# Kernel tuning notes

Hardware: AMD Instinct MI355X
Metric: run time of the kernel (lower is better)

The kernel has to match this reference:

```python
import jax, jax.numpy as jnp
import numpy as np

B, N, EMB, POS_EMB, ENC_DIM, NCLS, L = 256, 32, 128, 64, 256, 2, 4
EDGE_DIM = 2 * NCLS + 1            # one-hot(src) + one-hot(dst) + distance
IN_DIM = EMB + POS_EMB + 1         # enc_emb + pos_emb + numAgents_emb


def _w(k, shape):
    return jax.random.normal(k, shape, jnp.float32) / np.float32(np.sqrt(shape[-1]))


def setup_inputs() -> dict:
    key = jax.random.key(0)
    ks = jax.random.split(key, 16)
    return {
        "pos": jax.random.normal(ks[0], (B, N, 2), jnp.float32),
        "enc": jax.random.normal(ks[1], (B, ENC_DIM), jnp.float32),
        "pos_emb": jax.random.normal(ks[2], (B, N, POS_EMB), jnp.float32),
        "numAgents_emb": jax.random.normal(ks[3], (B, 1), jnp.float32),
        "T": jax.random.randint(ks[4], (B, N), 0, NCLS),
        "num_agents": N,
        # decoder_fc: Linear(ENC_DIM, EMB//2) -> Tanh -> Linear(EMB//2, EMB)
        "fc1_w": _w(ks[5], (EMB // 2, ENC_DIM)), "fc1_b": jnp.zeros((EMB // 2,), jnp.float32),
        "fc2_w": _w(ks[6], (EMB, EMB // 2)), "fc2_b": jnp.zeros((EMB,), jnp.float32),
        # lin_in: Linear(IN_DIM, EMB)
        "lin_w": _w(ks[7], (EMB, IN_DIM)), "lin_b": jnp.zeros((EMB,), jnp.float32),
        # per-layer message MLP: Linear(2*EMB+EDGE_DIM, EMB) -> Tanh -> Linear(EMB, EMB) -> Tanh
        "msg_w1": _w(ks[8], (L, EMB, 2 * EMB + EDGE_DIM)), "msg_b1": jnp.zeros((L, EMB), jnp.float32),
        "msg_w2": _w(ks[9], (L, EMB, EMB)), "msg_b2": jnp.zeros((L, EMB), jnp.float32),
        # per-layer update MLP: Linear(2*EMB, EMB) -> Tanh -> Linear(EMB, EMB) -> Tanh
        "upd_w1": _w(ks[10], (L, EMB, 2 * EMB)), "upd_b1": jnp.zeros((L, EMB), jnp.float32),
        "upd_w2": _w(ks[11], (L, EMB, EMB)), "upd_b2": jnp.zeros((L, EMB), jnp.float32),
    }


def reference(pos, enc, pos_emb, numAgents_emb, T, num_agents,
              fc1_w, fc1_b, fc2_w, fc2_b, lin_w, lin_b,
              msg_w1, msg_b1, msg_w2, msg_b2,
              upd_w1, upd_b1, upd_w2, upd_b2):
    b, n = pos.shape[0], num_agents
    # decoder_fc on scene encoding, broadcast to every agent (dropout in eval = identity)
    e = jnp.tanh(enc @ fc1_w.T + fc1_b) @ fc2_w.T + fc2_b            # (B, EMB)
    enc_emb = jnp.broadcast_to(e[:, None, :], (b, n, e.shape[-1]))
    na_emb = jnp.broadcast_to(numAgents_emb[:, None, :], (b, n, 1))
    x = jnp.concatenate([pos_emb, na_emb, enc_emb], axis=-1).reshape(b * n, -1)  # (B*N, IN_DIM)

    # fully connected edges per graph, batch-offset node ids
    row = jnp.repeat(jnp.arange(n), n)        # edge_index[0] = source j
    col = jnp.tile(jnp.arange(n), n)          # edge_index[1] = target i
    off = (jnp.arange(b) * n)[:, None]
    e_src = (row[None, :] + off).reshape(-1)  # (E,) with E = B*N^2
    e_dst = (col[None, :] + off).reshape(-1)

    # edge attributes: class one-hots of both endpoints + euclidean distance
    t_unique = jnp.arange(NCLS)
    T_oh = (T.reshape(-1)[:, None] == t_unique[None, :]).astype(jnp.float32)  # (B*N, NCLS)
    pf = pos.reshape(-1, 2)
    dist = jnp.sqrt(jnp.sum((pf[e_src] - pf[e_dst]) ** 2, axis=-1, keepdims=True))
    edge_attr = jnp.concatenate([T_oh[e_src], T_oh[e_dst], dist], axis=-1)     # (E, EDGE_DIM)

    # SocialInterDecGNN: lin_in, then L residual MPNN layers with add-aggregation
    h = x @ lin_w.T + lin_b
    for l in range(msg_w1.shape[0]):
        m_in = jnp.concatenate([h[e_dst], h[e_src], edge_attr], axis=-1)  # [h_i, h_j, e]
        m = jnp.tanh(jnp.tanh(m_in @ msg_w1[l].T + msg_b1[l]) @ msg_w2[l].T + msg_b2[l])
        aggr = jax.ops.segment_sum(m, e_dst, num_segments=b * n)          # scatter-add at target
        u_in = jnp.concatenate([h, aggr], axis=-1)
        h = h + jnp.tanh(jnp.tanh(u_in @ upd_w1[l].T + upd_b1[l]) @ upd_w2[l].T + upd_b2[l])
    return h  # (B*N, EMB)
```

## Files before the change

kernel.cpp:

```cpp
#include <hip/hip_runtime.h>

#define NN   32
#define EMB  128
#define PEMB 64
#define ENCD 256
#define NLAY 4
#define W1C  261
#define IND  193
#define UPAD 132
#define TSCALE 2.885390081777927f

typedef __attribute__((ext_vector_type(8))) short short8;
typedef __attribute__((ext_vector_type(4))) float floatx4;

__device__ unsigned short g_wC_h[16384 * 8], g_wC_l[16384 * 8];
__device__ unsigned short g_wD_h[8192 * 8],  g_wD_l[8192 * 8];
__device__ unsigned short g_wE1_h[16384 * 8], g_wE1_l[16384 * 8];
__device__ unsigned short g_wE2_h[8192 * 8],  g_wE2_l[8192 * 8];

__device__ __forceinline__ float fast_tanh(float x) {
  float e = __expf(2.0f * x);
  return 1.0f - __fdividef(2.0f, e + 1.0f);
}
__device__ __forceinline__ float tanh2(float s) {
  float e;
  asm("v_exp_f32 %0, %1" : "=v"(e) : "v"(s));
  const float ep1 = e + 1.0f;
  float r;
  asm("v_rcp_f32 %0, %1" : "=v"(r) : "v"(ep1));
  return __builtin_fmaf(-2.0f, r, 1.0f);
}
__device__ __forceinline__ unsigned short f2bf(float x) {
  unsigned u = __float_as_uint(x);
  return (unsigned short)((u + 0x7fffu + ((u >> 16) & 1u)) >> 16);
}
__device__ __forceinline__ float bf2f(unsigned short h) {
  return __uint_as_float(((unsigned)h) << 16);
}
__device__ __forceinline__ unsigned cvtpk(float a, float b) {
  unsigned r;
  asm("v_cvt_pk_bf16_f32 %0, %1, %2" : "=v"(r) : "v"(a), "v"(b));
  return r;
}

__device__ __forceinline__ floatx4 mfma3(short8 ah, short8 al, short8 bh, short8 bl, floatx4 acc) {
  acc = __builtin_amdgcn_mfma_f32_16x16x32_bf16(ah, bh, acc, 0, 0, 0);
  acc = __builtin_amdgcn_mfma_f32_16x16x32_bf16(al, bh, acc, 0, 0, 0);
  acc = __builtin_amdgcn_mfma_f32_16x16x32_bf16(ah, bl, acc, 0, 0, 0);
  return acc;
}

__device__ __forceinline__ void cvt_plane(const float (*src)[UPAD],
                                          unsigned short (*dH)[64][8],
                                          unsigned short (*dL)[64][8],
                                          int p, int lane) {
  const int row  = (lane & 15) + ((p & 1) << 4);
  const int koff = ((p >> 1) << 5) + ((lane >> 4) << 3);
  float x[8];
  *(float4*)&x[0] = *(const float4*)&src[row][koff];
  *(float4*)&x[4] = *(const float4*)&src[row][koff + 4];
  unsigned h[4], lo[4];
  #pragma unroll
  for (int q = 0; q < 4; q++) {
    h[q] = cvtpk(x[2*q], x[2*q+1]);
    const float r0 = x[2*q]   - __uint_as_float(h[q] << 16);
    const float r1 = x[2*q+1] - __uint_as_float(h[q] & 0xffff0000u);
    lo[q] = cvtpk(r0, r1);
  }
  *(uint4*)&dH[p][lane][0] = make_uint4(h[0], h[1], h[2], h[3]);
  *(uint4*)&dL[p][lane][0] = make_uint4(lo[0], lo[1], lo[2], lo[3]);
}

__device__ __forceinline__ short8 build_t(const float* uv, const float* vv,
                                          float d, const float* c5q) {
  float t[8];
  #pragma unroll
  for (int m = 0; m < 8; m++) t[m] = tanh2(uv[m] + vv[m] + d * c5q[m]);
  uint4 p = make_uint4(cvtpk(t[0], t[1]), cvtpk(t[2], t[3]),
                       cvtpk(t[4], t[5]), cvtpk(t[6], t[7]));
  return *(short8*)&p;
}

__device__ __forceinline__ float dot16_lds(const float* base, const float* wreg) {
  const float4 a = *(const float4*)(base);
  const float4 b = *(const float4*)(base + 4);
  const float4 c = *(const float4*)(base + 8);
  const float4 d = *(const float4*)(base + 12);
  return a.x*wreg[0] + a.y*wreg[1] + a.z*wreg[2]  + a.w*wreg[3]
       + b.x*wreg[4] + b.y*wreg[5] + b.z*wreg[6]  + b.w*wreg[7]
       + c.x*wreg[8] + c.y*wreg[9] + c.z*wreg[10] + c.w*wreg[11]
       + d.x*wreg[12]+ d.y*wreg[13]+ d.z*wreg[14] + d.w*wreg[15];
}

__global__ __launch_bounds__(256) void wconv(
    const float* __restrict__ msg_w1, const float* __restrict__ msg_w2,
    const float* __restrict__ upd_w1, const float* __restrict__ upd_w2) {
  const int t = blockIdx.x * 256 + threadIdx.x;
  const float* src;
  unsigned short *dh, *dl;
  if (t < 16384) {
    const int lane = t & 63, ks = (t >> 6) & 3, tile = (t >> 8) & 15, l = t >> 12;
    src = msg_w1 + l * EMB * W1C + (((tile & 7) << 4) + (lane & 15)) * W1C
        + (tile >> 3) * EMB + ks * 32 + ((lane >> 4) << 3);
    dh = g_wC_h + t * 8; dl = g_wC_l + t * 8;
  } else if (t < 24576) {
    const int r = t - 16384;
    const int lane = r & 63, ks = (r >> 6) & 3, ct = (r >> 8) & 7, l = r >> 11;
    src = msg_w2 + l * EMB * EMB + ((ct << 4) + (lane & 15)) * EMB + ks * 32 + ((lane >> 4) << 3);
    dh = g_wD_h + r * 8; dl = g_wD_l + r * 8;
  } else if (t < 40960) {
    const int r = t - 24576;
    const int lane = r & 63, ks = (r >> 6) & 7, ct = (r >> 9) & 7, l = r >> 12;
    src = upd_w1 + l * EMB * 2 * EMB + ((ct << 4) + (lane & 15)) * 2 * EMB + ks * 32 + ((lane >> 4) << 3);
    dh = g_wE1_h + r * 8; dl = g_wE1_l + r * 8;
  } else if (t < 49152) {
    const int r = t - 40960;
    const int lane = r & 63, ks = (r >> 6) & 3, ct = (r >> 8) & 7, l = r >> 11;
    src = upd_w2 + l * EMB * EMB + ((ct << 4) + (lane & 15)) * EMB + ks * 32 + ((lane >> 4) << 3);
    dh = g_wE2_h + r * 8; dl = g_wE2_l + r * 8;
  } else return;
  unsigned short hh[8], ll[8];
  #pragma unroll
  for (int m = 0; m < 8; m++) {
    const float x = src[m] * TSCALE;
    const unsigned short hb = f2bf(x);
    hh[m] = hb;
    ll[m] = f2bf(x - bf2f(hb));
  }
  *(short8*)dh = *(const short8*)hh;
  *(short8*)dl = *(const short8*)ll;
}

__global__ __launch_bounds__(1024)
__attribute__((amdgpu_waves_per_eu(4, 4)))
void fsd_fused(
    const float* __restrict__ pos, const float* __restrict__ enc,
    const float* __restrict__ pos_emb, const float* __restrict__ na_emb,
    const int* __restrict__ T,
    const float* __restrict__ fc1_w, const float* __restrict__ fc1_b,
    const float* __restrict__ fc2_w, const float* __restrict__ fc2_b,
    const float* __restrict__ lin_w, const float* __restrict__ lin_b,
    const float* __restrict__ msg_w1, const float* __restrict__ msg_b1,
    const float* __restrict__ msg_b2,
    const float* __restrict__ upd_b1, const float* __restrict__ upd_b2,
    float* __restrict__ out)
{
  __shared__ __align__(16) float h32[NN][UPAD];
  __shared__ __align__(16) float u_s[NN][UPAD];
  __shared__ __align__(16) float v_s[NN][UPAD];
  __shared__ __align__(16) unsigned short hfH[8][64][8],  hfL[8][64][8];
  __shared__ __align__(16) unsigned short agfH[8][64][8], agfL[8][64][8];
  __shared__ __align__(16) unsigned short w2fH[8][4][64][8], w2fL[8][4][64][8];
  __shared__ float e_s[EMB];
  __shared__ float c5_s[EMB];
  __shared__ float b2m_s[EMB];
  __shared__ float clsU[2][EMB], clsV[2][EMB];
  __shared__ float enc_s[ENCD];
  __shared__ float hidA_s[64];
  __shared__ float posx_s[NN], posy_s[NN];
  __shared__ int   T_s[NN];

  const int b    = blockIdx.x;
  const int tid  = threadIdx.x;
  const int w    = tid >> 6, lane = tid & 63;
  const int o    = tid & 127, g8 = tid >> 7;
  const int l15  = lane & 15, l4 = lane >> 4;

  if (tid < ENCD) enc_s[tid] = enc[b * ENCD + tid];
  if (tid < NN) {
    posx_s[tid] = pos[(b * NN + tid) * 2 + 0];
    posy_s[tid] = pos[(b * NN + tid) * 2 + 1];
    T_s[tid]    = T[b * NN + tid];
  }
  __syncthreads();
  if (tid < 64) {
    float a = fc1_b[tid];
    const float* wr = fc1_w + tid * ENCD;
    #pragma unroll 8
    for (int k = 0; k < ENCD; k++) a += enc_s[k] * wr[k];
    hidA_s[tid] = fast_tanh(a);
  }
  __syncthreads();
  if (tid < EMB) {
    float a = fc2_b[tid];
    const float* wr = fc2_w + tid * 64;
    #pragma unroll 8
    for (int k = 0; k < 64; k++) a += hidA_s[k] * wr[k];
    e_s[tid] = a;
  }
  float* pe_s = &u_s[0][0];
  for (int idx = tid; idx < NN * PEMB; idx += 1024)
    pe_s[idx] = pos_emb[b * NN * PEMB + idx];
  __syncthreads();

  {
    const float nav = na_emb[b];
    const float* wr = lin_w + o * IND;
    float ebias = lin_b[o] + nav * wr[PEMB];
    #pragma unroll 8
    for (int k = 0; k < EMB; k++) ebias += e_s[k] * wr[65 + k];
    float acc[4];
    #pragma unroll
    for (int n = 0; n < 4; n++) acc[n] = ebias;
    for (int kc = 0; kc < PEMB; kc += 16) {
      float wreg[16];
      #pragma unroll
      for (int q = 0; q < 16; q++) wreg[q] = wr[kc + q];
      #pragma unroll
      for (int n = 0; n < 4; n++)
        acc[n] += dot16_lds(&pe_s[(g8 + 8 * n) * PEMB + kc], wreg);
    }
    __syncthreads();
    #pragma unroll
    for (int n = 0; n < 4; n++) h32[g8 + 8 * n][o] = acc[n];
  }
  __syncthreads();
  if (w < 8) cvt_plane(h32, hfH, hfL, w, lane);
  __syncthreads();

  for (int l = 0; l < NLAY; l++) {
    const float* b1  = msg_b1 + l * EMB;
    const float* b2  = msg_b2 + l * EMB;
    const float* ub1 = upd_b1 + l * EMB;
    const float* ub2 = upd_b2 + l * EMB;
    const float* w1  = msg_w1 + l * EMB * W1C;

    if (tid < EMB) { c5_s[tid] = w1[tid * W1C + 260] * TSCALE; b2m_s[tid] = b2[tid] * TSCALE; }
    {
      const int c = (tid >> 7) & 1, oo = tid & 127;
      if (tid < 256)      clsU[c][oo] = (b1[oo] + w1[oo * W1C + 258 + c]) * TSCALE;
      else if (tid < 512) clsV[c][oo] = w1[oo * W1C + 256 + c] * TSCALE;
    }
    {
      const unsigned short* sH = g_wD_h + l * 16384;
      const unsigned short* sL = g_wD_l + l * 16384;
      unsigned short* dH = &w2fH[0][0][0][0];
      unsigned short* dL = &w2fL[0][0][0][0];
      for (int idx = tid; idx < 2048; idx += 1024) {
        *(short8*)(dH + idx * 8) = *(const short8*)(sH + idx * 8);
        *(short8*)(dL + idx * 8) = *(const short8*)(sL + idx * 8);
      }
    }
    __syncthreads();

    {
      const int part = w >> 3;
      const int col  = ((w & 7) << 4) + l15;
      floatx4 acc0 = {0.f,0.f,0.f,0.f}, acc1 = {0.f,0.f,0.f,0.f};
      #pragma unroll
      for (int ks = 0; ks < 4; ks++) {
        const int idx = (((l * 16 + w) * 4 + ks) * 64 + lane) * 8;
        const short8 bh = *(const short8*)(g_wC_h + idx);
        const short8 bl = *(const short8*)(g_wC_l + idx);
        const short8 ah0 = *(const short8*)&hfH[ks*2+0][lane][0];
        const short8 al0 = *(const short8*)&hfL[ks*2+0][lane][0];
        const short8 ah1 = *(const short8*)&hfH[ks*2+1][lane][0];
        const short8 al1 = *(const short8*)&hfL[ks*2+1][lane][0];
        acc0 = mfma3(ah0, al0, bh, bl, acc0);
        acc1 = mfma3(ah1, al1, bh, bl, acc1);
      }
      float (*dst)[UPAD] = part ? v_s : u_s;
      const float (*tab)[EMB] = part ? clsV : clsU;
      #pragma unroll
      for (int q = 0; q < 4; q++) {
        const int r0 = (l4 << 2) + q;
        const int r1 = r0 + 16;
        dst[r0][col] = acc0[q] + tab[T_s[r0]][col];
        dst[r1][col] = acc1[q] + tab[T_s[r1]][col];
      }
    }
    __syncthreads();

    {
      #pragma unroll 1
      for (int ii = 0; ii < 2; ii++) {
        const int i = (w << 1) + ii;
        const float pix = posx_s[i], piy = posy_s[i];
        float psum[8];
        #pragma unroll
        for (int ct = 0; ct < 8; ct++) psum[ct] = 0.f;

        #pragma unroll 1
        for (int jt = 0; jt < 2; jt++) {
          const int jr = l15 + (jt << 4);
          const float dxx = posx_s[jr] - pix, dyy = posy_s[jr] - piy;
          const float d = sqrtf(dxx * dxx + dyy * dyy);
          floatx4 acc[8];
          #pragma unroll
          for (int ct = 0; ct < 8; ct++) acc[ct] = (floatx4){0.f,0.f,0.f,0.f};

          #pragma unroll 1
          for (int q = 0; q < 4; q++) {
            const int k8 = (q << 5) + (l4 << 3);
            float uv[8], vv[8], c5q[8];
            *(float4*)&uv[0]  = *(const float4*)&u_s[i][k8];
            *(float4*)&uv[4]  = *(const float4*)&u_s[i][k8 + 4];
            *(float4*)&vv[0]  = *(const float4*)&v_s[jr][k8];
            *(float4*)&vv[4]  = *(const float4*)&v_s[jr][k8 + 4];
            *(float4*)&c5q[0] = *(const float4*)&c5_s[k8];
            *(float4*)&c5q[4] = *(const float4*)&c5_s[k8 + 4];
            const short8 aF = build_t(uv, vv, d, c5q);
            #pragma unroll
            for (int ct = 0; ct < 8; ct++) {
              const short8 bh = *(const short8*)&w2fH[ct][q][lane][0];
              const short8 bl = *(const short8*)&w2fL[ct][q][lane][0];
              acc[ct] = __builtin_amdgcn_mfma_f32_16x16x32_bf16(aF, bl, acc[ct], 0, 0, 0);
              acc[ct] = __builtin_amdgcn_mfma_f32_16x16x32_bf16(aF, bh, acc[ct], 0, 0, 0);
            }
          }
          #pragma unroll
          for (int ct = 0; ct < 8; ct++) {
            const float b2c = b2m_s[(ct << 4) + l15];
            #pragma unroll
            for (int q = 0; q < 4; q++)
              psum[ct] += tanh2(acc[ct][q] + b2c);
          }
        }

        #pragma unroll
        for (int ct = 0; ct < 8; ct++) {
          float p = psum[ct];
          p += __shfl_xor(p, 16);
          p += __shfl_xor(p, 32);
          if (lane < 16) {
            const int c     = (ct << 4) + l15;
            const int plane = ((c >> 5) << 1) + (i >> 4);
            const int slot  = (i & 15) + (((c >> 3) & 3) << 4);
            const int elem  = c & 7;
            const unsigned short hb = f2bf(p);
            agfH[plane][slot][elem] = hb;
            agfL[plane][slot][elem] = f2bf(p - bf2f(hb));
          }
        }
      }
    }
    __syncthreads();

    {
      const int ct = w & 7, jt = w >> 3;
      const int col = (ct << 4) + l15;
      const float bo = ub1[col] * TSCALE;
      floatx4 acc = {0.f,0.f,0.f,0.f};
      #pragma unroll
      for (int ks = 0; ks < 8; ks++) {
        const int idx = (((l * 8 + ct) * 8 + ks) * 64 + lane) * 8;
        const short8 bh = *(const short8*)(g_wE1_h + idx);
        const short8 bl = *(const short8*)(g_wE1_l + idx);
        short8 ah, al;
        if (ks < 4) {
          ah = *(const short8*)&hfH[ks*2+jt][lane][0];
          al = *(const short8*)&hfL[ks*2+jt][lane][0];
        } else {
          ah = *(const short8*)&agfH[(ks-4)*2+jt][lane][0];
          al = *(const short8*)&agfL[(ks-4)*2+jt][lane][0];
        }
        acc = mfma3(ah, al, bh, bl, acc);
      }
      #pragma unroll
      for (int q = 0; q < 4; q++) {
        const int r = (jt << 4) + (l4 << 2) + q;
        u_s[r][col] = tanh2(acc[q] + bo);
      }
    }
    __syncthreads();

    if (w < 8) cvt_plane(u_s, agfH, agfL, w, lane);
    __syncthreads();

    {
      const int ct = w & 7, jt = w >> 3;
      const int col = (ct << 4) + l15;
      const float bo = ub2[col] * TSCALE;
      floatx4 acc = {0.f,0.f,0.f,0.f};
      #pragma unroll
      for (int ks = 0; ks < 4; ks++) {
        const int idx = (((l * 8 + ct) * 4 + ks) * 64 + lane) * 8;
        const short8 bh = *(const short8*)(g_wE2_h + idx);
        const short8 bl = *(const short8*)(g_wE2_l + idx);
        const short8 ah = *(const short8*)&agfH[ks*2+jt][lane][0];
        const short8 al = *(const short8*)&agfL[ks*2+jt][lane][0];
        acc = mfma3(ah, al, bh, bl, acc);
      }
      #pragma unroll
      for (int q = 0; q < 4; q++) {
        const int r = (jt << 4) + (l4 << 2) + q;
        h32[r][col] += tanh2(acc[q] + bo);
      }
    }
    __syncthreads();

    if (l + 1 < NLAY) {
      if (w < 8) cvt_plane(h32, hfH, hfL, w, lane);
      __syncthreads();
    }
  }

  for (int idx = tid; idx < NN * EMB; idx += 1024)
    out[b * NN * EMB + idx] = h32[idx >> 7][idx & 127];
}

extern "C" void kernel_launch(void* const* d_in, const int* in_sizes, int n_in,
                              void* d_out, int out_size, void* d_ws, size_t ws_size,
                              hipStream_t stream) {
  const float* pos     = (const float*)d_in[0];
  const float* enc     = (const float*)d_in[1];
  const float* pos_emb = (const float*)d_in[2];
  const float* na_emb  = (const float*)d_in[3];
  const int*   T       = (const int*)d_in[4];
  const float* fc1_w = (const float*)d_in[6];
  const float* fc1_b = (const float*)d_in[7];
  const float* fc2_w = (const float*)d_in[8];
  const float* fc2_b = (const float*)d_in[9];
  const float* lin_w = (const float*)d_in[10];
  const float* lin_b = (const float*)d_in[11];
  const float* msg_w1 = (const float*)d_in[12];
  const float* msg_b1 = (const float*)d_in[13];
  const float* msg_w2 = (const float*)d_in[14];
  const float* msg_b2 = (const float*)d_in[15];
  const float* upd_w1 = (const float*)d_in[16];
  const float* upd_b1 = (const float*)d_in[17];
  const float* upd_w2 = (const float*)d_in[18];
  const float* upd_b2 = (const float*)d_in[19];

  wconv<<<192, 256, 0, stream>>>(msg_w1, msg_w2, upd_w1, upd_w2);
  fsd_fused<<<256, 1024, 0, stream>>>(pos, enc, pos_emb, na_emb, T,
      fc1_w, fc1_b, fc2_w, fc2_b, lin_w, lin_b,
      msg_w1, msg_b1, msg_b2, upd_b1, upd_b2,
      (float*)d_out);
}
```

Measured before the change: 171.0 us.

## Switch edge message second-layer GEMM to 32x32x16 MFMA tiles

Reorganizes the per-edge message MLP second layer to use 32x32x16 bf16 MFMA instead of 16x16x32, with each wave covering all 32 source agents at once. The msg_w2 fragment layout in wconv and in LDS is reordered to match, the tanh-input A fragments are built once per target agent and reused across four output column tiles, and sched_group_barrier hints interleave LDS reads with MFMAs. This is meant to cut redundant A-fragment construction, LDS traffic and the cross-lane reduction. In exchange it holds more registers (16-wide accumulators plus eight A fragments), which may strain occupancy at the fixed waves-per-EU setting.

```diff
diff --git a/kernel.cpp b/kernel.cpp
--- a/kernel.cpp
+++ b/kernel.cpp
@@ -12,6 +12,7 @@
 
 typedef __attribute__((ext_vector_type(8))) short short8;
 typedef __attribute__((ext_vector_type(4))) float floatx4;
+typedef __attribute__((ext_vector_type(16))) float floatx16;
 
 __device__ unsigned short g_wC_h[16384 * 8], g_wC_l[16384 * 8];
 __device__ unsigned short g_wD_h[8192 * 8],  g_wD_l[8192 * 8];
@@ -71,13 +72,20 @@
   *(uint4*)&dL[p][lane][0] = make_uint4(lo[0], lo[1], lo[2], lo[3]);
 }
 
-__device__ __forceinline__ short8 build_t(const float* uv, const float* vv,
-                                          float d, const float* c5q) {
-  float t[8];
-  #pragma unroll
-  for (int m = 0; m < 8; m++) t[m] = tanh2(uv[m] + vv[m] + d * c5q[m]);
-  uint4 p = make_uint4(cvtpk(t[0], t[1]), cvtpk(t[2], t[3]),
-                       cvtpk(t[4], t[5]), cvtpk(t[6], t[7]));
+__device__ __forceinline__ short8 build_t32(const float* us, const float* vs,
+                                            const float* cs, float d) {
+  const float4 u0 = *(const float4*)us, u1 = *(const float4*)(us + 4);
+  const float4 v0 = *(const float4*)vs, v1 = *(const float4*)(vs + 4);
+  const float4 c0 = *(const float4*)cs, c1 = *(const float4*)(cs + 4);
+  const float t0 = tanh2(u0.x + v0.x + d * c0.x);
+  const float t1 = tanh2(u0.y + v0.y + d * c0.y);
+  const float t2 = tanh2(u0.z + v0.z + d * c0.z);
+  const float t3 = tanh2(u0.w + v0.w + d * c0.w);
+  const float t4 = tanh2(u1.x + v1.x + d * c1.x);
+  const float t5 = tanh2(u1.y + v1.y + d * c1.y);
+  const float t6 = tanh2(u1.z + v1.z + d * c1.z);
+  const float t7 = tanh2(u1.w + v1.w + d * c1.w);
+  uint4 p = make_uint4(cvtpk(t0, t1), cvtpk(t2, t3), cvtpk(t4, t5), cvtpk(t6, t7));
   return *(short8*)&p;
 }
 
@@ -105,8 +113,8 @@
     dh = g_wC_h + t * 8; dl = g_wC_l + t * 8;
   } else if (t < 24576) {
     const int r = t - 16384;
-    const int lane = r & 63, ks = (r >> 6) & 3, ct = (r >> 8) & 7, l = r >> 11;
-    src = msg_w2 + l * EMB * EMB + ((ct << 4) + (lane & 15)) * EMB + ks * 32 + ((lane >> 4) << 3);
+    const int lane = r & 63, kt = (r >> 6) & 7, nt = (r >> 9) & 3, l = r >> 11;
+    src = msg_w2 + l * EMB * EMB + ((nt << 5) + (lane & 31)) * EMB + (kt << 4) + ((lane >> 5) << 3);
     dh = g_wD_h + r * 8; dl = g_wD_l + r * 8;
   } else if (t < 40960) {
     const int r = t - 24576;
@@ -150,7 +158,7 @@
   __shared__ __align__(16) float v_s[NN][UPAD];
   __shared__ __align__(16) unsigned short hfH[8][64][8],  hfL[8][64][8];
   __shared__ __align__(16) unsigned short agfH[8][64][8], agfL[8][64][8];
-  __shared__ __align__(16) unsigned short w2fH[8][4][64][8], w2fL[8][4][64][8];
+  __shared__ __align__(16) unsigned short w2fH[4][8][64][8], w2fL[4][8][64][8];
   __shared__ float e_s[EMB];
   __shared__ float c5_s[EMB];
   __shared__ float b2m_s[EMB];
@@ -272,59 +280,52 @@
     __syncthreads();
 
     {
+      const int j32 = lane & 31;
+      const int khi = (lane >> 5) << 3;
+      const float pjx = posx_s[j32], pjy = posy_s[j32];
       #pragma unroll 1
       for (int ii = 0; ii < 2; ii++) {
         const int i = (w << 1) + ii;
-        const float pix = posx_s[i], piy = posy_s[i];
-        float psum[8];
-        #pragma unroll
-        for (int ct = 0; ct < 8; ct++) psum[ct] = 0.f;
+        const float dxx = pjx - posx_s[i], dyy = pjy - posy_s[i];
+        const float d = sqrtf(dxx * dxx + dyy * dyy);
+        const short8 aF0 = build_t32(&u_s[i][  0 + khi], &v_s[j32][  0 + khi], &c5_s[  0 + khi], d);
+        const short8 aF1 = build_t32(&u_s[i][ 16 + khi], &v_s[j32][ 16 + khi], &c5_s[ 16 + khi], d);
+        const short8 aF2 = build_t32(&u_s[i][ 32 + khi], &v_s[j32][ 32 + khi], &c5_s[ 32 + khi], d);
+        const short8 aF3 = build_t32(&u_s[i][ 48 + khi], &v_s[j32][ 48 + khi], &c5_s[ 48 + khi], d);
+        const short8 aF4 = build_t32(&u_s[i][ 64 + khi], &v_s[j32][ 64 + khi], &c5_s[ 64 + khi], d);
+        const short8 aF5 = build_t32(&u_s[i][ 80 + khi], &v_s[j32][ 80 + khi], &c5_s[ 80 + khi], d);
+        const short8 aF6 = build_t32(&u_s[i][ 96 + khi], &v_s[j32][ 96 + khi], &c5_s[ 96 + khi], d);
+        const short8 aF7 = build_t32(&u_s[i][112 + khi], &v_s[j32][112 + khi], &c5_s[112 + khi], d);
 
         #pragma unroll 1
-        for (int jt = 0; jt < 2; jt++) {
-          const int jr = l15 + (jt << 4);
-          const float dxx = posx_s[jr] - pix, dyy = posy_s[jr] - piy;
-          const float d = sqrtf(dxx * dxx + dyy * dyy);
-          floatx4 acc[8];
+        for (int nt = 0; nt < 4; nt++) {
+          floatx16 acc = {0.f,0.f,0.f,0.f,0.f,0.f,0.f,0.f,0.f,0.f,0.f,0.f,0.f,0.f,0.f,0.f};
+          #define DSTEP(kt, aF) { \
+            const short8 bl_ = *(const short8*)&w2fL[nt][kt][lane][0]; \
+            acc = __builtin_amdgcn_mfma_f32_32x32x16_bf16(aF, bl_, acc, 0, 0, 0); \
+            const short8 bh_ = *(const short8*)&w2fH[nt][kt][lane][0]; \
+            acc = __builtin_amdgcn_mfma_f32_32x32x16_bf16(aF, bh_, acc, 0, 0, 0); }
+          DSTEP(0, aF0) DSTEP(1, aF1) DSTEP(2, aF2) DSTEP(3, aF3)
+          DSTEP(4, aF4) DSTEP(5, aF5) DSTEP(6, aF6) DSTEP(7, aF7)
+          #undef DSTEP
           #pragma unroll
-          for (int ct = 0; ct < 8; ct++) acc[ct] = (floatx4){0.f,0.f,0.f,0.f};
-
-          #pragma unroll 1
-          for (int q = 0; q < 4; q++) {
-            const int k8 = (q << 5) + (l4 << 3);
-            float uv[8], vv[8], c5q[8];
-            *(float4*)&uv[0]  = *(const float4*)&u_s[i][k8];
-            *(float4*)&uv[4]  = *(const float4*)&u_s[i][k8 + 4];
-            *(float4*)&vv[0]  = *(const float4*)&v_s[jr][k8];
-            *(float4*)&vv[4]  = *(const float4*)&v_s[jr][k8 + 4];
-            *(float4*)&c5q[0] = *(const float4*)&c5_s[k8];
-            *(float4*)&c5q[4] = *(const float4*)&c5_s[k8 + 4];
-            const short8 aF = build_t(uv, vv, d, c5q);
-            #pragma unroll
-            for (int ct = 0; ct < 8; ct++) {
-              const short8 bh = *(const short8*)&w2fH[ct][q][lane][0];
-              const short8 bl = *(const short8*)&w2fL[ct][q][lane][0];
-              acc[ct] = __builtin_amdgcn_mfma_f32_16x16x32_bf16(aF, bl, acc[ct], 0, 0, 0);
-              acc[ct] = __builtin_amdgcn_mfma_f32_16x16x32_bf16(aF, bh, acc[ct], 0, 0, 0);
-            }
+          for (int g = 0; g < 16; g++) {
+            __builtin_amdgcn_sched_group_barrier(0x100, 1, 0);
+            __builtin_amdgcn_sched_group_barrier(0x008, 1, 0);
           }
+          __builtin_amdgcn_sched_barrier(0);
+          const int c = (nt << 5) + j32;
+          const float b2c = b2m_s[c];
+          float p0 = 0.f, p1 = 0.f;
           #pragma unroll
-          for (int ct = 0; ct < 8; ct++) {
-            const float b2c = b2m_s[(ct << 4) + l15];
-            #pragma unroll
-            for (int q = 0; q < 4; q++)
-              psum[ct] += tanh2(acc[ct][q] + b2c);
+          for (int rr = 0; rr < 16; rr += 2) {
+            p0 += tanh2(acc[rr]     + b2c);
+            p1 += tanh2(acc[rr + 1] + b2c);
           }
-        }
-
-        #pragma unroll
-        for (int ct = 0; ct < 8; ct++) {
-          float p = psum[ct];
-          p += __shfl_xor(p, 16);
+          float p = p0 + p1;
           p += __shfl_xor(p, 32);
-          if (lane < 16) {
-            const int c     = (ct << 4) + l15;
-            const int plane = ((c >> 5) << 1) + (i >> 4);
+          if (lane < 32) {
+            const int plane = (nt << 1) + (i >> 4);
             const int slot  = (i & 15) + (((c >> 3) & 3) << 4);
             const int elem  = c & 7;
             const unsigned short hb = f2bf(p);
```

New measurement: 161.7 us. 5.4% less time.
